# Kernel tuning notes

Hardware: AMD Instinct MI355X
Metric: run time of the kernel (lower is better)

Reference implementation:

```python
import jax, jax.numpy as jnp
import numpy as np

B, S, E, O, LAYERS = 256, 28, 256, 256, 3


def setup_inputs() -> dict:
    key = jax.random.key(0)
    ks = jax.random.split(key, 20)
    sc = 0.05
    inp = {
        "centers": jax.random.normal(ks[0], (B, S, 3), jnp.float32),
        "object_embedding": jax.random.normal(ks[1], (B, S, E), jnp.float32),
        "counts": jax.random.randint(ks[2], (B,), 1, S + 1),
        # linear_relation_object: 3 -> E
        "Wr": jax.random.normal(ks[3], (E, 3), jnp.float32) * sc,
        "br": jnp.zeros((E,), jnp.float32),
        # LSTM (PyTorch gate order i,f,g,o)
        "W_ih": jax.random.normal(ks[4], (4 * O, E), jnp.float32) * sc,
        "W_hh": jax.random.normal(ks[5], (4 * O, O), jnp.float32) * sc,
        "b_ih": jnp.zeros((4 * O,), jnp.float32),
        "b_hh": jnp.zeros((4 * O,), jnp.float32),
        # gr: 3E -> O
        "Wgr": jax.random.normal(ks[6], (O, 3 * E), jnp.float32) * sc,
        "bgr": jnp.zeros((O,), jnp.float32),
        # bezier control: O -> O, plus scalar alpha
        "Wbc": jax.random.normal(ks[7], (O, O), jnp.float32) * sc,
        "bbc": jnp.zeros((O,), jnp.float32),
        "alpha": jnp.asarray(0.5, jnp.float32),
        # esa: E -> O
        "Wesa": jax.random.normal(ks[8], (O, E), jnp.float32) * sc,
        "besa": jnp.zeros((O,), jnp.float32),
        # gaussian heads: O -> 3
        "Wmu": jax.random.normal(ks[9], (3, O), jnp.float32) * sc,
        "bmu": jnp.zeros((3,), jnp.float32),
        "Wlv": jax.random.normal(ks[10], (3, O), jnp.float32) * sc,
        "blv": jnp.zeros((3,), jnp.float32),
    }
    return inp


def _lstm(x, W_ih, W_hh, b_ih, b_hh):
    # x: [B,S,E] -> hs: [B,S,O], zero initial state, PyTorch gate order i,f,g,o
    Bdim = x.shape[0]
    Odim = W_hh.shape[1]
    b = b_ih + b_hh

    def step(carry, xt):
        h, c = carry
        z = xt @ W_ih.T + h @ W_hh.T + b  # [B,4O]
        i, f, g, o = jnp.split(z, 4, axis=-1)
        c = jax.nn.sigmoid(f) * c + jax.nn.sigmoid(i) * jnp.tanh(g)
        h = jax.nn.sigmoid(o) * jnp.tanh(c)
        return (h, c), h

    h0 = jnp.zeros((Bdim, Odim), x.dtype)
    _, hs = jax.lax.scan(step, (h0, h0), jnp.swapaxes(x, 0, 1))
    return jnp.swapaxes(hs, 0, 1)


def reference(centers, object_embedding, counts, Wr, br, W_ih, W_hh, b_ih, b_hh,
              Wgr, bgr, Wbc, bbc, alpha, Wesa, besa, Wmu, bmu, Wlv, blv):
    # masks from per-scene object counts (padding replication of the torch loops)
    idx = jnp.arange(S)
    obj_mask = (idx[None, :] < counts[:, None]).astype(jnp.float32)[..., None]  # [B,S,1]
    rel_mask = (obj_mask[:, :, None, :] * obj_mask[:, None, :, :])              # [B,S,S,1]

    centers_p = centers * obj_mask                     # padded centers are zero
    relation = centers_p[:, :, None, :] - centers_p[:, None, :, :]  # [B,S,S,3]
    rlf = relation @ Wr.T + br                         # [B,S,S,E]

    olf = object_embedding * obj_mask                  # [B,S,E]
    t = jax.nn.sigmoid(alpha)

    for _ in range(LAYERS):
        new_olf = _lstm(olf, W_ih, W_hh, b_ih, b_hh) * obj_mask
        rep_i = jnp.broadcast_to(olf[:, :, None, :], (olf.shape[0], S, S, olf.shape[-1]))
        rep_j = jnp.broadcast_to(olf[:, None, :, :], (olf.shape[0], S, S, olf.shape[-1]))
        cat = jnp.concatenate([rep_i, rep_j, rlf], axis=-1)   # [B,S,S,3E]
        rlf_lin = cat @ Wgr.T + bgr                           # [B,S,S,O]
        cp = rlf_lin @ Wbc.T + bbc
        bez = ((1 - t) ** 2 + t ** 2) * rlf_lin + 2 * (1 - t) * t * cp
        rlf = jnp.tanh(bez) * rel_mask
        olf = new_olf

    rlf = rlf @ Wesa.T + besa                                  # [B,S,S,O]
    # base attention: softmax over dim=1 (explicit max-subtract as in source)
    base_attn = jax.nn.softmax(rlf - jnp.max(rlf, axis=1, keepdims=True), axis=1)
    # gaussian attention (eval mode: eps = 0 -> samples = mus)
    mus = rlf @ Wmu.T + bmu                                    # [B,S,S,3]
    _logvars = rlf @ Wlv.T + blv                               # computed, unused at eval
    gscores = jnp.mean(mus, axis=-1, keepdims=True)            # [B,S,S,1]
    gattn = jax.nn.softmax(gscores, axis=1)
    attn = 0.5 * base_attn + 0.5 * gattn                       # broadcast over O
    rel_out = jnp.sum(attn * rlf, axis=-2) * obj_mask          # [B,S,O]
    return rel_out
```

## Files before the change

### kernel.cpp

```cpp
#include <hip/hip_runtime.h>


typedef __attribute__((ext_vector_type(8))) short short8;
typedef __attribute__((ext_vector_type(4))) float f32x4;

__device__ __forceinline__ float b2f(unsigned short u){
  union { unsigned int i; float f; } v; v.i = ((unsigned int)u) << 16; return v.f;
}
__device__ __forceinline__ float u2f(unsigned int u){
  union { unsigned int i; float f; } v; v.i = u; return v.f;
}
__device__ __forceinline__ unsigned short f2b(float f){
  union { float f; unsigned int i; } v; v.f = f;
  return (unsigned short)((v.i + 0x8000u) >> 16);
}
__device__ __forceinline__ unsigned int pk2(float lo, float hi){
  union { float f; unsigned int i; } a, b; a.f = lo; b.f = hi;
  return ((a.i + 0x8000u) >> 16) | ((b.i + 0x8000u) & 0xffff0000u);
}
__device__ __forceinline__ float sigm(float x){ return 1.f/(1.f+__expf(-x)); }
__device__ __forceinline__ float tanh_f(float x){ float e = __expf(2.f*x); return 1.f - 2.f/(e+1.f); }
__device__ __forceinline__ int xsw(int row, int n){
  int c = n >> 3;
  int pc = (c & 24) | ((c ^ row) & 7);
  return row*256 + pc*8 + (n & 7);
}

#define MFMA16(a,b,c) __builtin_amdgcn_mfma_f32_16x16x32_bf16((a),(b),(c),0,0,0)

__global__ __launch_bounds__(256) void k_repack7(const float* __restrict__ Wih,
                                                 const float* __restrict__ Whh,
                                                 const float* __restrict__ Wgr,
                                                 const float* __restrict__ Wbc,
                                                 const float* __restrict__ Wesa,
                                                 const float* __restrict__ Wmu,
                                                 unsigned short* __restrict__ wcv,
                                                 float* __restrict__ wmean){
  int i = blockIdx.x*256 + threadIdx.x;
  if (i >= 851968){
    int o = i - 851968;
    if (o < 256) wmean[o] = (Wmu[o] + Wmu[256+o] + Wmu[512+o]) * (1.f/3.f);
    return;
  }
  const float* s; int segbase, N, stride, off, local;
  if      (i < 262144){ s=Wih;  segbase=0;      N=1024; stride=256; off=0;   local=i; }
  else if (i < 524288){ s=Whh;  segbase=262144; N=1024; stride=256; off=0;   local=i-262144; }
  else if (i < 589824){ s=Wgr;  segbase=524288; N=256;  stride=768; off=0;   local=i-524288; }
  else if (i < 655360){ s=Wgr;  segbase=589824; N=256;  stride=768; off=256; local=i-589824; }
  else if (i < 720896){ s=Wgr;  segbase=655360; N=256;  stride=768; off=512; local=i-655360; }
  else if (i < 786432){ s=Wbc;  segbase=720896; N=256;  stride=256; off=0;   local=i-720896; }
  else                { s=Wesa; segbase=786432; N=256;  stride=256; off=0;   local=i-786432; }
  int n = local >> 8, k = local & 255;
  wcv[segbase + (((k >> 3)*N + n) << 3) + (k & 7)] = f2b(s[n*stride + off + k]);
}

__global__ __launch_bounds__(256) void k_prep(const float* __restrict__ emb,
                                              const int* __restrict__ counts,
                                              unsigned short* __restrict__ olf,
                                              float* __restrict__ out){
  int bs = blockIdx.x;
  int b = bs / 28; int s = bs - b*28;
  int e = threadIdx.x;
  olf[(size_t)bs*256 + e] = (s < counts[b]) ? f2b(emb[(size_t)bs*256 + e]) : (unsigned short)0;
  out[(size_t)bs*256 + e] = 0.f;
}

__global__ __launch_bounds__(256) void k_xgemm(const unsigned short* __restrict__ olf,
                                               const unsigned short* __restrict__ Wih,
                                               unsigned short* __restrict__ zx){
  const int tid = threadIdx.x;
  const int wid = tid >> 6, lane = tid & 63, col = lane & 15, quad = lane >> 4;
  const int m0 = (blockIdx.x >> 1)*64 + wid*16;
  const int nt0 = (blockIdx.x & 1)*32;
  short8 af[8];
  #pragma unroll
  for (int kt=0; kt<8; ++kt)
    af[kt] = *(const short8*)&olf[(size_t)(m0 + col)*256 + kt*32 + quad*8];
  #pragma unroll 4
  for (int nt=nt0; nt<nt0+32; ++nt){
    int n = nt*16 + col;
    f32x4 acc = (f32x4){0.f,0.f,0.f,0.f};
    #pragma unroll
    for (int kt=0; kt<8; ++kt){
      short8 bf = *(const short8*)&Wih[((((kt*4 + quad) << 10) + n) << 3)];
      acc = MFMA16(af[kt], bf, acc);
    }
    #pragma unroll
    for (int r=0; r<4; ++r)
      zx[(size_t)(m0 + quad*4 + r)*1024 + n] = f2b(acc[r]);
  }
}

__global__ __launch_bounds__(1024) void k_recat(const unsigned short* __restrict__ zx,
                                                const unsigned short* __restrict__ Whh,
                                                const float* __restrict__ bih,
                                                const float* __restrict__ bhh,
                                                const int* __restrict__ counts,
                                                unsigned short* __restrict__ olf_out,
                                                const unsigned short* __restrict__ olf_at,
                                                const unsigned short* __restrict__ Wgri,
                                                const unsigned short* __restrict__ Wgrj,
                                                unsigned short* __restrict__ At_out){
  __shared__ unsigned short Ab[2][16*264];
  const int tid = threadIdx.x;
  const int wv = tid >> 6, lane = tid & 63, col = lane & 15, quad = lane >> 4;

  if (blockIdx.x >= 16){
    const int m0 = (blockIdx.x - 16)*256 + wv*16;
    short8 af[8];
    #pragma unroll
    for (int kt=0; kt<8; ++kt)
      af[kt] = *(const short8*)&olf_at[(size_t)(m0 + col)*256 + kt*32 + quad*8];
    #pragma unroll 4
    for (int nt=0; nt<32; ++nt){
      const unsigned short* wb = (nt < 16) ? Wgri : Wgrj;
      int nn = (nt & 15)*16 + col;
      f32x4 acc = (f32x4){0.f,0.f,0.f,0.f};
      #pragma unroll
      for (int kt=0; kt<8; ++kt){
        short8 bf = *(const short8*)&wb[((((kt*4 + quad) << 8) + nn) << 3)];
        acc = MFMA16(af[kt], bf, acc);
      }
      #pragma unroll
      for (int r=0; r<4; ++r)
        At_out[(size_t)(m0 + quad*4 + r)*512 + nt*16 + col] = f2b(acc[r]);
    }
    return;
  }
  const int sc0 = blockIdx.x * 16;
  const int u = wv*16 + col;
  float bz[4];
  #pragma unroll
  for (int g=0; g<4; ++g) bz[g] = bih[g*256+u] + bhh[g*256+u];
  int cnt4[4];
  #pragma unroll
  for (int r=0; r<4; ++r) cnt4[r] = counts[sc0 + quad*4 + r];

  float cst[4];
  #pragma unroll
  for (int r=0; r<4; ++r) cst[r] = 0.f;
  for (int i=tid; i<16*264; i+=1024) Ab[0][i] = 0;
  __syncthreads();

  for (int t=0; t<28; ++t){
    const int cur = t & 1, nxt = cur ^ 1;
    float zxv[4][4];
    #pragma unroll
    for (int g=0; g<4; ++g){
      #pragma unroll
      for (int r=0; r<4; ++r)
        zxv[g][r] = b2f(zx[((size_t)(sc0 + quad*4 + r)*28 + t)*1024 + g*256 + u]);
    }
    f32x4 acc[4];
    #pragma unroll
    for (int g=0; g<4; ++g) acc[g] = (f32x4){0.f,0.f,0.f,0.f};
    #pragma unroll
    for (int kt=0; kt<8; ++kt){
      short8 a = *(const short8*)&Ab[cur][col*264 + kt*32 + quad*8];
      #pragma unroll
      for (int g=0; g<4; ++g){
        short8 bf = *(const short8*)&Whh[((((kt*4 + quad) << 10) + g*256 + u) << 3)];
        acc[g] = MFMA16(a, bf, acc[g]);
      }
    }
    #pragma unroll
    for (int r=0; r<4; ++r){
      int s = quad*4 + r;
      float zi = acc[0][r] + zxv[0][r] + bz[0];
      float zf = acc[1][r] + zxv[1][r] + bz[1];
      float zg = acc[2][r] + zxv[2][r] + bz[2];
      float zo = acc[3][r] + zxv[3][r] + bz[3];
      float cc = sigm(zf)*cst[r] + sigm(zi)*tanh_f(zg);
      cst[r] = cc;
      float hh = sigm(zo)*tanh_f(cc);
      unsigned short hb = f2b(hh);
      Ab[nxt][s*264 + u] = hb;
      olf_out[((size_t)(sc0+s)*28 + t)*256 + u] = (t < cnt4[r]) ? hb : (unsigned short)0;
    }
    __syncthreads();
  }
}

__global__ __launch_bounds__(256) void k_aterm(const unsigned short* __restrict__ olf,
                                               const unsigned short* __restrict__ Wgri,
                                               const unsigned short* __restrict__ Wgrj,
                                               unsigned short* __restrict__ Aout){
  const int tid = threadIdx.x;
  const int wid = tid >> 6, lane = tid & 63, col = lane & 15, quad = lane >> 4;
  const int m0 = blockIdx.x*64 + wid*16;
  short8 af[8];
  #pragma unroll
  for (int kt=0; kt<8; ++kt)
    af[kt] = *(const short8*)&olf[(size_t)(m0 + col)*256 + kt*32 + quad*8];
  #pragma unroll 4
  for (int nt=0; nt<32; ++nt){
    const unsigned short* wb = (nt < 16) ? Wgri : Wgrj;
    int nn = (nt & 15)*16 + col;
    f32x4 acc = (f32x4){0.f,0.f,0.f,0.f};
    #pragma unroll
    for (int kt=0; kt<8; ++kt){
      short8 bf = *(const short8*)&wb[((((kt*4 + quad) << 8) + nn) << 3)];
      acc = MFMA16(af[kt], bf, acc);
    }
    #pragma unroll
    for (int r=0; r<4; ++r)
      Aout[(size_t)(m0 + quad*4 + r)*512 + nt*16 + col] = f2b(acc[r]);
  }
}

#define GEMM_TILE64(SRC, WPTR)                                                      \
  {                                                                                 \
    _Pragma("unroll")                                                               \
    for (int rf=0; rf<4; ++rf){ Ya[rf][0]=(f32x4){0.f,0.f,0.f,0.f};                 \
                                Ya[rf][1]=(f32x4){0.f,0.f,0.f,0.f}; }               \
    _Pragma("unroll 1")                                                             \
    for (int kc=0; kc<4; ++kc){                                                     \
      short8 av[2][4], bv[2][2];                                                    \
      _Pragma("unroll")                                                             \
      for (int u=0; u<2; ++u){                                                      \
        int kt = kc*2 + u;                                                          \
        _Pragma("unroll")                                                           \
        for (int rf=0; rf<4; ++rf)                                                  \
          av[u][rf] = *(const short8*)&(SRC)[(Abase[rf] + kc*64) ^ (u*32)];         \
        bv[u][0] = *(const short8*)&(WPTR)[Bbase + kt*8192];                        \
        bv[u][1] = *(const short8*)&(WPTR)[Bbase + kt*8192 + 128];                  \
      }                                                                             \
      __builtin_amdgcn_s_setprio(1);                                                \
      _Pragma("unroll")                                                             \
      for (int u=0; u<2; ++u){                                                      \
        _Pragma("unroll")                                                           \
        for (int rf=0; rf<4; ++rf){                                                 \
          Ya[rf][0] = MFMA16(bv[u][0], av[u][rf], Ya[rf][0]);                       \
          Ya[rf][1] = MFMA16(bv[u][1], av[u][rf], Ya[rf][1]);                       \
        }                                                                           \
      }                                                                             \
      __builtin_amdgcn_s_setprio(0);                                                \
    }                                                                               \
  }

__global__ __launch_bounds__(512) void k_mega(
    const float* __restrict__ centers, const int* __restrict__ counts,
    const float* __restrict__ Wr, const float* __restrict__ br,
    const unsigned short* __restrict__ Wgrr, const float* __restrict__ bgr,
    const unsigned short* __restrict__ Wbc, const float* __restrict__ bbc,
    const float* __restrict__ alpha,
    const unsigned short* __restrict__ Wesa, const float* __restrict__ besa,
    const float* __restrict__ wmean, const float* __restrict__ bmu,
    const unsigned short* __restrict__ Aterm, float* __restrict__ out){
  __shared__ unsigned short Xa[64*256];
  __shared__ unsigned short Yb[64*256];
  float* hrSBp = (float*)&Xa[56*256];
  float* gsbp  = (float*)&Xa[60*256];
  float* hrSGp = (float*)&Xa[60*256+128];
  const int tid = threadIdx.x;
  const int wv = tid >> 6;
  const int lane = tid & 63, col = lane & 15, quad = lane >> 4;
  const int xcd = blockIdx.x & 7, idx = blockIdx.x >> 3;
  const int b = xcd*32 + idx/14, jt = idx - (idx/14)*14;
  const int cb = counts[b];
  const int nbase = wv*32;

  float av_ = alpha[0];
  float tv = sigm(av_);
  float c1 = (1.f-tv)*(1.f-tv) + tv*tv;
  float c2 = 2.f*tv*(1.f-tv);

  float pv[4];
  const unsigned short* apI[4];
  const unsigned short* apJ[4];
  #pragma unroll
  for (int mt=0; mt<4; ++mt){
    int m = mt*16 + col;
    int i = m >> 1;
    int pi = (i < 27) ? i : 27;
    int pj = jt*2 + (m & 1);
    pv[mt] = (m < 56 && i < cb && pj < cb) ? 1.f : 0.f;
    apI[mt] = Aterm + (size_t)(b*28 + pi)*512 + nbase + quad*4;
    apJ[mt] = Aterm + (size_t)(b*28 + pj)*512 + 256 + nbase + quad*4;
  }
  int Abase[4];
  #pragma unroll
  for (int rf=0; rf<4; ++rf){
    int row = rf*16 + col;
    Abase[rf] = row*256 + ((quad ^ (row & 3)) | (row & 4))*8;
  }
  const int Bbase = (quad*256 + nbase + col)*8;
  int woff[4][2];
  f32x4 bgv[2], bbv[2], bev[2];
  #pragma unroll
  for (int nt2=0; nt2<2; ++nt2){
    int n0 = nbase + nt2*16 + quad*4;
    bgv[nt2] = *(const f32x4*)&bgr[n0];
    bbv[nt2] = *(const f32x4*)&bbc[n0];
    bev[nt2] = *(const f32x4*)&besa[n0];
    #pragma unroll
    for (int mt=0; mt<4; ++mt)
      woff[mt][nt2] = xsw(mt*16 + col, n0);
  }

  {
    int m = tid >> 3, sub = tid & 7;
    int i = m >> 1, j = jt*2 + (m & 1);
    bool valid = (m < 56);
    float mi = (valid && i < cb) ? 1.f : 0.f;
    float mj = (valid && j < cb) ? 1.f : 0.f;
    float vm = valid ? 1.f : 0.f;
    const float* ci = centers + (b*28 + (valid ? i : 0))*3;
    const float* cj = centers + (b*28 + j)*3;
    float dx = mi*ci[0] - mj*cj[0];
    float dy = mi*ci[1] - mj*cj[1];
    float dz = mi*ci[2] - mj*cj[2];
    #pragma unroll
    for (int c8=0; c8<4; ++c8){
      int e0 = sub*32 + c8*8;
      f32x4 w0 = *(const f32x4*)&Wr[e0*3 +  0];
      f32x4 w1 = *(const f32x4*)&Wr[e0*3 +  4];
      f32x4 w2 = *(const f32x4*)&Wr[e0*3 +  8];
      f32x4 w3 = *(const f32x4*)&Wr[e0*3 + 12];
      f32x4 w4 = *(const f32x4*)&Wr[e0*3 + 16];
      f32x4 w5 = *(const f32x4*)&Wr[e0*3 + 20];
      f32x4 b0 = *(const f32x4*)&br[e0];
      f32x4 b1 = *(const f32x4*)&br[e0+4];
      b0 *= vm; b1 *= vm;
      float v0 = dx*w0[0] + dy*w0[1] + dz*w0[2] + b0[0];
      float v1 = dx*w0[3] + dy*w1[0] + dz*w1[1] + b0[1];
      float v2 = dx*w1[2] + dy*w1[3] + dz*w2[0] + b0[2];
      float v3 = dx*w2[1] + dy*w2[2] + dz*w2[3] + b0[3];
      float v4 = dx*w3[0] + dy*w3[1] + dz*w3[2] + b1[0];
      float v5 = dx*w3[3] + dy*w4[0] + dz*w4[1] + b1[1];
      float v6 = dx*w4[2] + dy*w4[3] + dz*w5[0] + b1[2];
      float v7 = dx*w5[1] + dy*w5[2] + dz*w5[3] + b1[3];
      uint4 pw;
      pw.x = pk2(v0,v1); pw.y = pk2(v2,v3); pw.z = pk2(v4,v5); pw.w = pk2(v6,v7);
      *(uint4*)&Xa[xsw(m, e0)] = pw;
    }
  }
  __syncthreads();

  f32x4 Ya[4][2];
  #pragma unroll 1
  for (int l=0; l<3; ++l){
    uint2 rAi[4][2], rAj[4][2];
    #pragma unroll
    for (int mt=0; mt<4; ++mt){
      rAi[mt][0] = *(const uint2*)&apI[mt][0];
      rAi[mt][1] = *(const uint2*)&apI[mt][16];
      rAj[mt][0] = *(const uint2*)&apJ[mt][0];
      rAj[mt][1] = *(const uint2*)&apJ[mt][16];
      apI[mt] += 7168*512; apJ[mt] += 7168*512;
    }
    GEMM_TILE64(Xa, Wgrr);
    #pragma unroll
    for (int nt2=0; nt2<2; ++nt2){
      #pragma unroll
      for (int mt=0; mt<4; ++mt){
        uint2 wi = rAi[mt][nt2], wj = rAj[mt][nt2];
        float v0 = Ya[mt][nt2][0] + bgv[nt2][0] + u2f(wi.x << 16)         + u2f(wj.x << 16);
        float v1 = Ya[mt][nt2][1] + bgv[nt2][1] + u2f(wi.x & 0xffff0000u) + u2f(wj.x & 0xffff0000u);
        float v2 = Ya[mt][nt2][2] + bgv[nt2][2] + u2f(wi.y << 16)         + u2f(wj.y << 16);
        float v3 = Ya[mt][nt2][3] + bgv[nt2][3] + u2f(wi.y & 0xffff0000u) + u2f(wj.y & 0xffff0000u);
        *(uint2*)&Yb[woff[mt][nt2]] = make_uint2(pk2(v0,v1), pk2(v2,v3));
      }
    }
    __syncthreads();
    GEMM_TILE64(Yb, Wbc);
    #pragma unroll
    for (int nt2=0; nt2<2; ++nt2){
      #pragma unroll
      for (int mt=0; mt<4; ++mt){
        uint2 w = *(const uint2*)&Yb[woff[mt][nt2]];
        float r0 = u2f(w.x << 16),         r1 = u2f(w.x & 0xffff0000u);
        float r2 = u2f(w.y << 16),         r3 = u2f(w.y & 0xffff0000u);
        float x0 = tanh_f(c1*r0 + c2*(Ya[mt][nt2][0] + bbv[nt2][0])) * pv[mt];
        float x1 = tanh_f(c1*r1 + c2*(Ya[mt][nt2][1] + bbv[nt2][1])) * pv[mt];
        float x2 = tanh_f(c1*r2 + c2*(Ya[mt][nt2][2] + bbv[nt2][2])) * pv[mt];
        float x3 = tanh_f(c1*r3 + c2*(Ya[mt][nt2][3] + bbv[nt2][3])) * pv[mt];
        *(uint2*)&Xa[woff[mt][nt2]] = make_uint2(pk2(x0,x1), pk2(x2,x3));
      }
    }
    __syncthreads();
  }
  GEMM_TILE64(Xa, Wesa);
  __syncthreads();
  #pragma unroll
  for (int nt2=0; nt2<2; ++nt2){
    #pragma unroll
    for (int mt=0; mt<4; ++mt){
      float v0 = Ya[mt][nt2][0] + bev[nt2][0];
      float v1 = Ya[mt][nt2][1] + bev[nt2][1];
      float v2 = Ya[mt][nt2][2] + bev[nt2][2];
      float v3 = Ya[mt][nt2][3] + bev[nt2][3];
      *(uint2*)&Yb[woff[mt][nt2]] = make_uint2(pk2(v0,v1), pk2(v2,v3));
      *(uint2*)&Xa[woff[mt][nt2]] =
          make_uint2(pk2(__expf(v0),__expf(v1)), pk2(__expf(v2),__expf(v3)));
    }
  }
  __syncthreads();
  {
    int m = tid >> 3, sub = tid & 7;
    if (m < 56){
      float s = 0.f;
      #pragma unroll
      for (int c8=0; c8<4; ++c8){
        int e0 = sub*32 + c8*8;
        uint4 u = *(const uint4*)&Yb[xsw(m, e0)];
        f32x4 wm0 = *(const f32x4*)&wmean[e0];
        f32x4 wm1 = *(const f32x4*)&wmean[e0+4];
        s += u2f(u.x << 16)*wm0[0] + u2f(u.x & 0xffff0000u)*wm0[1]
           + u2f(u.y << 16)*wm0[2] + u2f(u.y & 0xffff0000u)*wm0[3]
           + u2f(u.z << 16)*wm1[0] + u2f(u.z & 0xffff0000u)*wm1[1]
           + u2f(u.w << 16)*wm1[2] + u2f(u.w & 0xffff0000u)*wm1[3];
      }
      s += __shfl_xor(s, 1, 64);
      s += __shfl_xor(s, 2, 64);
      s += __shfl_xor(s, 4, 64);
      if (sub == 0)
        gsbp[m] = __expf(s + (bmu[0] + bmu[1] + bmu[2])*(1.f/3.f));
    }
  }
  {
    int jc = tid >> 8, o = tid & 255;
    float se = 0.f;
    #pragma unroll
    for (int i=0;i<28;++i) se += b2f(Xa[xsw(i*2+jc, o)]);
    hrSBp[jc*256 + o] = 0.5f / se;
  }
  __syncthreads();
  if (tid < 2){
    int jc = tid;
    float se = 0.f;
    for (int i=0;i<28;++i) se += gsbp[i*2+jc];
    hrSGp[jc] = 0.5f / se;
  }
  __syncthreads();
  for (int it = tid; it < 7168; it += 512){
    int i = it >> 8, o = it & 255;
    if (i < cb){
      float s = 0.f;
      #pragma unroll
      for (int jc=0; jc<2; ++jc){
        int row = i*2 + jc;
        int off = xsw(row, o);
        float v = b2f(Yb[off]);
        float E = b2f(Xa[off]);
        float a = E*hrSBp[jc*256+o] + gsbp[row]*hrSGp[jc];
        s += a * v;
      }
      atomicAdd(&out[((size_t)b*28 + i)*256 + o], s);
    }
  }
}

extern "C" void kernel_launch(void* const* d_in, const int* in_sizes, int n_in,
                              void* d_out, int out_size, void* d_ws, size_t ws_size,
                              hipStream_t stream){
  const float* centers = (const float*)d_in[0];
  const float* emb     = (const float*)d_in[1];
  const int*   counts  = (const int*)d_in[2];
  const float* Wr      = (const float*)d_in[3];
  const float* br      = (const float*)d_in[4];
  const float* Wih     = (const float*)d_in[5];
  const float* Whh     = (const float*)d_in[6];
  const float* bih     = (const float*)d_in[7];
  const float* bhh     = (const float*)d_in[8];
  const float* Wgr     = (const float*)d_in[9];
  const float* bgr     = (const float*)d_in[10];
  const float* Wbc     = (const float*)d_in[11];
  const float* bbc     = (const float*)d_in[12];
  const float* alpha   = (const float*)d_in[13];
  const float* Wesa    = (const float*)d_in[14];
  const float* besa    = (const float*)d_in[15];
  const float* Wmu     = (const float*)d_in[16];
  const float* bmu     = (const float*)d_in[17];

  unsigned short* olf   = (unsigned short*)d_ws;
  unsigned short* At    = (unsigned short*)((char*)d_ws + 11010048);
  unsigned short* zx    = (unsigned short*)((char*)d_ws + 33030144);
  unsigned short* wcv   = (unsigned short*)((char*)d_ws + 47710208);
  float*          wmean = (float*)((char*)d_ws + 49414144);
  unsigned short* cWih  = wcv;
  unsigned short* cWhh  = wcv + 262144;
  unsigned short* cWgri = wcv + 524288;
  unsigned short* cWgrj = wcv + 589824;
  unsigned short* cWgrr = wcv + 655360;
  unsigned short* cWbc  = wcv + 720896;
  unsigned short* cWesa = wcv + 786432;
  float* outp = (float*)d_out;

  unsigned short* olf1 = olf + (size_t)7168*256;
  unsigned short* olf2 = olf + (size_t)2*7168*256;
  unsigned short* At1  = At  + (size_t)7168*512;
  unsigned short* At2  = At  + (size_t)2*7168*512;

  hipLaunchKernelGGL(k_repack7, dim3(3329), dim3(256), 0, stream,
                     Wih, Whh, Wgr, Wbc, Wesa, Wmu, wcv, wmean);
  hipLaunchKernelGGL(k_prep, dim3(7168), dim3(256), 0, stream, emb, counts, olf, outp);
  hipLaunchKernelGGL(k_xgemm, dim3(224), dim3(256), 0, stream, olf, cWih, zx);
  hipLaunchKernelGGL(k_recat, dim3(44), dim3(1024), 0, stream,
                     zx, cWhh, bih, bhh, counts, olf1, olf, cWgri, cWgrj, At);
  hipLaunchKernelGGL(k_xgemm, dim3(224), dim3(256), 0, stream, olf1, cWih, zx);
  hipLaunchKernelGGL(k_recat, dim3(44), dim3(1024), 0, stream,
                     zx, cWhh, bih, bhh, counts, olf2, olf1, cWgri, cWgrj, At1);
  hipLaunchKernelGGL(k_aterm, dim3(112), dim3(256), 0, stream, olf2, cWgri, cWgrj, At2);
  hipLaunchKernelGGL(k_mega,  dim3(3584), dim3(512), 0, stream,
                     centers, counts, Wr, br, cWgrr, bgr, cWbc, bbc, alpha,
                     cWesa, besa, wmean, bmu, At, outp);
}
```

Baseline: 1.232 ms.

## Fold bias into A-term GEMMs, compute softmax sums in registers, vectorize epilogue

Result: faster. 1.185 ms (-3.8%).

```diff
diff --git a/kernel.cpp b/kernel.cpp
--- a/kernel.cpp
+++ b/kernel.cpp
@@ -16,7 +16,7 @@
 }
 __device__ __forceinline__ unsigned int pk2(float lo, float hi){
   union { float f; unsigned int i; } a, b; a.f = lo; b.f = hi;
-  return ((a.i + 0x8000u) >> 16) | ((b.i + 0x8000u) & 0xffff0000u);
+  return __builtin_amdgcn_perm(b.i + 0x8000u, a.i + 0x8000u, 0x07060302u);
 }
 __device__ __forceinline__ float sigm(float x){ return 1.f/(1.f+__expf(-x)); }
 __device__ __forceinline__ float tanh_f(float x){ float e = __expf(2.f*x); return 1.f - 2.f/(e+1.f); }
@@ -100,6 +100,7 @@
                                                 const unsigned short* __restrict__ olf_at,
                                                 const unsigned short* __restrict__ Wgri,
                                                 const unsigned short* __restrict__ Wgrj,
+                                                const float* __restrict__ bgr,
                                                 unsigned short* __restrict__ At_out){
   __shared__ unsigned short Ab[2][16*264];
   const int tid = threadIdx.x;
@@ -115,6 +116,7 @@
     for (int nt=0; nt<32; ++nt){
       const unsigned short* wb = (nt < 16) ? Wgri : Wgrj;
       int nn = (nt & 15)*16 + col;
+      float bg = (nt < 16) ? bgr[nn] : 0.f;
       f32x4 acc = (f32x4){0.f,0.f,0.f,0.f};
       #pragma unroll
       for (int kt=0; kt<8; ++kt){
@@ -123,7 +125,7 @@
       }
       #pragma unroll
       for (int r=0; r<4; ++r)
-        At_out[(size_t)(m0 + quad*4 + r)*512 + nt*16 + col] = f2b(acc[r]);
+        At_out[(size_t)(m0 + quad*4 + r)*512 + nt*16 + col] = f2b(acc[r] + bg);
     }
     return;
   }
@@ -184,6 +186,7 @@
 __global__ __launch_bounds__(256) void k_aterm(const unsigned short* __restrict__ olf,
                                                const unsigned short* __restrict__ Wgri,
                                                const unsigned short* __restrict__ Wgrj,
+                                               const float* __restrict__ bgr,
                                                unsigned short* __restrict__ Aout){
   const int tid = threadIdx.x;
   const int wid = tid >> 6, lane = tid & 63, col = lane & 15, quad = lane >> 4;
@@ -196,6 +199,7 @@
   for (int nt=0; nt<32; ++nt){
     const unsigned short* wb = (nt < 16) ? Wgri : Wgrj;
     int nn = (nt & 15)*16 + col;
+    float bg = (nt < 16) ? bgr[nn] : 0.f;
     f32x4 acc = (f32x4){0.f,0.f,0.f,0.f};
     #pragma unroll
     for (int kt=0; kt<8; ++kt){
@@ -204,7 +208,7 @@
     }
     #pragma unroll
     for (int r=0; r<4; ++r)
-      Aout[(size_t)(m0 + quad*4 + r)*512 + nt*16 + col] = f2b(acc[r]);
+      Aout[(size_t)(m0 + quad*4 + r)*512 + nt*16 + col] = f2b(acc[r] + bg);
   }
 }
 
@@ -238,7 +242,7 @@
     }                                                                               \
   }
 
-__global__ __launch_bounds__(512) void k_mega(
+__global__ __launch_bounds__(512, 4) void k_mega(
     const float* __restrict__ centers, const int* __restrict__ counts,
     const float* __restrict__ Wr, const float* __restrict__ br,
     const unsigned short* __restrict__ Wgrr, const float* __restrict__ bgr,
@@ -286,12 +290,11 @@
   }
   const int Bbase = (quad*256 + nbase + col)*8;
   int woff[4][2];
-  f32x4 bgv[2], bbv[2], bev[2];
+  f32x4 cbb[2], bev[2];
   #pragma unroll
   for (int nt2=0; nt2<2; ++nt2){
     int n0 = nbase + nt2*16 + quad*4;
-    bgv[nt2] = *(const f32x4*)&bgr[n0];
-    bbv[nt2] = *(const f32x4*)&bbc[n0];
+    cbb[nt2] = (*(const f32x4*)&bbc[n0]) * c2;
     bev[nt2] = *(const f32x4*)&besa[n0];
     #pragma unroll
     for (int mt=0; mt<4; ++mt)
@@ -355,11 +358,13 @@
       #pragma unroll
       for (int mt=0; mt<4; ++mt){
         uint2 wi = rAi[mt][nt2], wj = rAj[mt][nt2];
-        float v0 = Ya[mt][nt2][0] + bgv[nt2][0] + u2f(wi.x << 16)         + u2f(wj.x << 16);
-        float v1 = Ya[mt][nt2][1] + bgv[nt2][1] + u2f(wi.x & 0xffff0000u) + u2f(wj.x & 0xffff0000u);
-        float v2 = Ya[mt][nt2][2] + bgv[nt2][2] + u2f(wi.y << 16)         + u2f(wj.y << 16);
-        float v3 = Ya[mt][nt2][3] + bgv[nt2][3] + u2f(wi.y & 0xffff0000u) + u2f(wj.y & 0xffff0000u);
-        *(uint2*)&Yb[woff[mt][nt2]] = make_uint2(pk2(v0,v1), pk2(v2,v3));
+        f32x4 ai, aj;
+        ai[0] = u2f(wi.x << 16); ai[1] = u2f(wi.x & 0xffff0000u);
+        ai[2] = u2f(wi.y << 16); ai[3] = u2f(wi.y & 0xffff0000u);
+        aj[0] = u2f(wj.x << 16); aj[1] = u2f(wj.x & 0xffff0000u);
+        aj[2] = u2f(wj.y << 16); aj[3] = u2f(wj.y & 0xffff0000u);
+        f32x4 v = Ya[mt][nt2] + ai + aj;
+        *(uint2*)&Yb[woff[mt][nt2]] = make_uint2(pk2(v[0],v[1]), pk2(v[2],v[3]));
       }
     }
     __syncthreads();
@@ -369,12 +374,15 @@
       #pragma unroll
       for (int mt=0; mt<4; ++mt){
         uint2 w = *(const uint2*)&Yb[woff[mt][nt2]];
-        float r0 = u2f(w.x << 16),         r1 = u2f(w.x & 0xffff0000u);
-        float r2 = u2f(w.y << 16),         r3 = u2f(w.y & 0xffff0000u);
-        float x0 = tanh_f(c1*r0 + c2*(Ya[mt][nt2][0] + bbv[nt2][0])) * pv[mt];
-        float x1 = tanh_f(c1*r1 + c2*(Ya[mt][nt2][1] + bbv[nt2][1])) * pv[mt];
-        float x2 = tanh_f(c1*r2 + c2*(Ya[mt][nt2][2] + bbv[nt2][2])) * pv[mt];
-        float x3 = tanh_f(c1*r3 + c2*(Ya[mt][nt2][3] + bbv[nt2][3])) * pv[mt];
+        f32x4 rl;
+        rl[0] = u2f(w.x << 16); rl[1] = u2f(w.x & 0xffff0000u);
+        rl[2] = u2f(w.y << 16); rl[3] = u2f(w.y & 0xffff0000u);
+        f32x4 bez = Ya[mt][nt2]*c2 + cbb[nt2];
+        bez = rl*c1 + bez;
+        float x0 = tanh_f(bez[0]) * pv[mt];
+        float x1 = tanh_f(bez[1]) * pv[mt];
+        float x2 = tanh_f(bez[2]) * pv[mt];
+        float x3 = tanh_f(bez[3]) * pv[mt];
         *(uint2*)&Xa[woff[mt][nt2]] = make_uint2(pk2(x0,x1), pk2(x2,x3));
       }
     }
@@ -382,17 +390,33 @@
   }
   GEMM_TILE64(Xa, Wesa);
   __syncthreads();
+  f32x4 sbp[2] = {(f32x4){0.f,0.f,0.f,0.f}, (f32x4){0.f,0.f,0.f,0.f}};
+  const float m3f = (col < 8) ? 1.f : 0.f;
   #pragma unroll
   for (int nt2=0; nt2<2; ++nt2){
     #pragma unroll
     for (int mt=0; mt<4; ++mt){
-      float v0 = Ya[mt][nt2][0] + bev[nt2][0];
-      float v1 = Ya[mt][nt2][1] + bev[nt2][1];
-      float v2 = Ya[mt][nt2][2] + bev[nt2][2];
-      float v3 = Ya[mt][nt2][3] + bev[nt2][3];
-      *(uint2*)&Yb[woff[mt][nt2]] = make_uint2(pk2(v0,v1), pk2(v2,v3));
-      *(uint2*)&Xa[woff[mt][nt2]] =
-          make_uint2(pk2(__expf(v0),__expf(v1)), pk2(__expf(v2),__expf(v3)));
+      f32x4 v = Ya[mt][nt2] + bev[nt2];
+      *(uint2*)&Yb[woff[mt][nt2]] = make_uint2(pk2(v[0],v[1]), pk2(v[2],v[3]));
+      f32x4 e;
+      e[0] = __expf(v[0]); e[1] = __expf(v[1]);
+      e[2] = __expf(v[2]); e[3] = __expf(v[3]);
+      *(uint2*)&Xa[woff[mt][nt2]] = make_uint2(pk2(e[0],e[1]), pk2(e[2],e[3]));
+      f32x4 wsum = e;
+      if (mt == 3) wsum *= m3f;
+      sbp[nt2] += wsum;
+    }
+  }
+  f32x4 hr[2];
+  #pragma unroll
+  for (int nt2=0; nt2<2; ++nt2){
+    #pragma unroll
+    for (int r=0; r<4; ++r){
+      float s = sbp[nt2][r];
+      s += __shfl_xor(s, 2, 64);
+      s += __shfl_xor(s, 4, 64);
+      s += __shfl_xor(s, 8, 64);
+      hr[nt2][r] = 0.5f / s;
     }
   }
   __syncthreads();
@@ -418,12 +442,13 @@
         gsbp[m] = __expf(s + (bmu[0] + bmu[1] + bmu[2])*(1.f/3.f));
     }
   }
-  {
-    int jc = tid >> 8, o = tid & 255;
-    float se = 0.f;
-    #pragma unroll
-    for (int i=0;i<28;++i) se += b2f(Xa[xsw(i*2+jc, o)]);
-    hrSBp[jc*256 + o] = 0.5f / se;
+  if (col < 2){
+    #pragma unroll
+    for (int nt2=0; nt2<2; ++nt2){
+      #pragma unroll
+      for (int r=0; r<4; ++r)
+        hrSBp[col*256 + nbase + nt2*16 + quad*4 + r] = hr[nt2][r];
+    }
   }
   __syncthreads();
   if (tid < 2){
@@ -433,20 +458,32 @@
     hrSGp[jc] = 0.5f / se;
   }
   __syncthreads();
-  for (int it = tid; it < 7168; it += 512){
-    int i = it >> 8, o = it & 255;
+  for (int it = tid; it < 1792; it += 512){
+    int i = it >> 6, og = (it & 63)*4;
     if (i < cb){
-      float s = 0.f;
+      f32x4 s = (f32x4){0.f,0.f,0.f,0.f};
       #pragma unroll
       for (int jc=0; jc<2; ++jc){
         int row = i*2 + jc;
-        int off = xsw(row, o);
-        float v = b2f(Yb[off]);
-        float E = b2f(Xa[off]);
-        float a = E*hrSBp[jc*256+o] + gsbp[row]*hrSGp[jc];
-        s += a * v;
+        int off = xsw(row, og);
+        uint2 yw = *(const uint2*)&Yb[off];
+        uint2 xw = *(const uint2*)&Xa[off];
+        f32x4 hb = *(const f32x4*)&hrSBp[jc*256 + og];
+        float gg = gsbp[row]*hrSGp[jc];
+        float vv0 = u2f(yw.x << 16), vv1 = u2f(yw.x & 0xffff0000u);
+        float vv2 = u2f(yw.y << 16), vv3 = u2f(yw.y & 0xffff0000u);
+        float E0 = u2f(xw.x << 16),  E1 = u2f(xw.x & 0xffff0000u);
+        float E2 = u2f(xw.y << 16),  E3 = u2f(xw.y & 0xffff0000u);
+        s[0] += (E0*hb[0] + gg)*vv0;
+        s[1] += (E1*hb[1] + gg)*vv1;
+        s[2] += (E2*hb[2] + gg)*vv2;
+        s[3] += (E3*hb[3] + gg)*vv3;
       }
-      atomicAdd(&out[((size_t)b*28 + i)*256 + o], s);
+      float* op = &out[((size_t)b*28 + i)*256 + og];
+      atomicAdd(&op[0], s[0]);
+      atomicAdd(&op[1], s[1]);
+      atomicAdd(&op[2], s[2]);
+      atomicAdd(&op[3], s[3]);
     }
   }
 }
@@ -497,11 +534,11 @@
   hipLaunchKernelGGL(k_prep, dim3(7168), dim3(256), 0, stream, emb, counts, olf, outp);
   hipLaunchKernelGGL(k_xgemm, dim3(224), dim3(256), 0, stream, olf, cWih, zx);
   hipLaunchKernelGGL(k_recat, dim3(44), dim3(1024), 0, stream,
-                     zx, cWhh, bih, bhh, counts, olf1, olf, cWgri, cWgrj, At);
+                     zx, cWhh, bih, bhh, counts, olf1, olf, cWgri, cWgrj, bgr, At);
   hipLaunchKernelGGL(k_xgemm, dim3(224), dim3(256), 0, stream, olf1, cWih, zx);
   hipLaunchKernelGGL(k_recat, dim3(44), dim3(1024), 0, stream,
-                     zx, cWhh, bih, bhh, counts, olf2, olf1, cWgri, cWgrj, At1);
-  hipLaunchKernelGGL(k_aterm, dim3(112), dim3(256), 0, stream, olf2, cWgri, cWgrj, At2);
+                     zx, cWhh, bih, bhh, counts, olf2, olf1, cWgri, cWgrj, bgr, At1);
+  hipLaunchKernelGGL(k_aterm, dim3(112), dim3(256), 0, stream, olf2, cWgri, cWgrj, bgr, At2);
   hipLaunchKernelGGL(k_mega,  dim3(3584), dim3(512), 0, stream,
                      centers, counts, Wr, br, cWgrr, bgr, cWbc, bbc, alpha,
                      cWesa, besa, wmean, bmu, At, outp);
```
